# Kernel optimization log

Hardware: AMD Instinct MI355X
Metric: run time of the kernel (lower is better)

The kernel has to match this reference:

```python
import jax, jax.numpy as jnp
import numpy as np

N_NODES = 100000
N_EDGES = 640000
D_IN = 128
D_HID = 128
D_OUT = 128
EPS = 1e-12  # F.normalize clamp_min eps


def _sage_conv(x, src, dst, Wl, bl, Wr):
    # mean aggregation of source features onto destination nodes
    msgs = x[src]                                              # [E, C] gather
    agg = jax.ops.segment_sum(msgs, dst, num_segments=N_NODES)  # [N, C] scatter-add
    cnt = jax.ops.segment_sum(jnp.ones((src.shape[0],), x.dtype), dst,
                              num_segments=N_NODES)
    agg = agg / jnp.maximum(cnt, 1.0)[:, None]
    out = agg @ Wl.T + bl + x @ Wr.T                           # lin_l(aggr) + lin_r(root)
    # L2 row-normalize (normalize=True)
    norm = jnp.sqrt(jnp.sum(out * out, axis=-1, keepdims=True))
    return out / jnp.maximum(norm, EPS)


def setup_inputs() -> dict:
    key = jax.random.key(0)
    ks = jax.random.split(key, 8)
    x = jax.random.normal(ks[0], (N_NODES, D_IN), dtype=jnp.float32)
    edge_index = jax.random.randint(ks[1], (2, N_EDGES), 0, N_NODES, dtype=jnp.int64)
    s1 = 1.0 / np.sqrt(D_IN)
    s2 = 1.0 / np.sqrt(D_HID)
    Wl1 = jax.random.uniform(ks[2], (D_HID, D_IN), jnp.float32, -s1, s1)
    bl1 = jax.random.uniform(ks[3], (D_HID,), jnp.float32, -s1, s1)
    Wr1 = jax.random.uniform(ks[4], (D_HID, D_IN), jnp.float32, -s1, s1)
    Wl2 = jax.random.uniform(ks[5], (D_OUT, D_HID), jnp.float32, -s2, s2)
    bl2 = jax.random.uniform(ks[6], (D_OUT,), jnp.float32, -s2, s2)
    Wr2 = jax.random.uniform(ks[7], (D_OUT, D_HID), jnp.float32, -s2, s2)
    return {"x": x, "edge_index": edge_index, "Wl1": Wl1, "bl1": bl1,
            "Wr1": Wr1, "Wl2": Wl2, "bl2": bl2, "Wr2": Wr2}


def reference(x, edge_index, Wl1, bl1, Wr1, Wl2, bl2, Wr2):
    src, dst = edge_index[0], edge_index[1]
    h = _sage_conv(x, src, dst, Wl1, bl1, Wr1)
    h = jax.nn.relu(h)  # dropout is identity in eval mode
    h = _sage_conv(h, src, dst, Wl2, bl2, Wr2)
    return h
```

## Files before the change

### kernel.cpp

```cpp
#include <hip/hip_runtime.h>
#include <hip/hip_bf16.h>
#include <stdint.h>

#define N_NODES 100000
#define N_EDGES 640000
#define MPAD    100096
#define CONV_T  (N_NODES * 64)
#define EDGE_BLOCKS ((N_EDGES + 255) / 256)

typedef short  bf8_t  __attribute__((ext_vector_type(8)));
typedef float  f32x4  __attribute__((ext_vector_type(4)));

__device__ __forceinline__ unsigned f2bf(float f) {
  unsigned u = __builtin_bit_cast(unsigned, f);
  return ((u + 0x7fffu + ((u >> 16) & 1u)) >> 16) & 0xffffu;
}
__device__ __forceinline__ float bf2f(unsigned bits) {
  return __builtin_bit_cast(float, bits << 16);
}

__global__ void k_count_prep(const int* __restrict__ dst, int* __restrict__ cnt,
                             const float* __restrict__ x, unsigned* __restrict__ A1,
                             const float* __restrict__ Wl1, const float* __restrict__ Wr1,
                             unsigned short* __restrict__ Bf1,
                             const float* __restrict__ Wl2, const float* __restrict__ Wr2,
                             unsigned short* __restrict__ Bf2) {
  if (blockIdx.x < EDGE_BLOCKS) {
    int e = blockIdx.x * 256 + threadIdx.x;
    if (e < N_EDGES) atomicAdd(&cnt[dst[e]], 1);
    return;
  }
  int i = (blockIdx.x - EDGE_BLOCKS) * 256 + threadIdx.x;
  if (i < CONV_T) {
    int w = i >> 6, lane = i & 63;
    float2 v = ((const float2*)x)[i];
    A1[(size_t)w * 128 + 64 + lane] = f2bf(v.x) | (f2bf(v.y) << 16);
    return;
  }
  int gid = i - CONV_T;
  if (gid >= 8192) return;
  int tid = gid & 4095;
  const float* Wl = (gid < 4096) ? Wl1 : Wl2;
  const float* Wr = (gid < 4096) ? Wr1 : Wr2;
  unsigned short* Bf = (gid < 4096) ? Bf1 : Bf2;
  int lane = tid & 63;
  int t  = (tid >> 6) & 7;
  int kc = tid >> 9;
  int c = lane & 15, q = lane >> 4;
  int col = t * 16 + c;
  for (int j = 0; j < 8; ++j) {
    int k = kc * 32 + q * 8 + j;
    float v = (k < 128) ? Wl[col * 128 + k] : Wr[col * 128 + (k - 128)];
    Bf[(size_t)tid * 8 + j] = (unsigned short)f2bf(v);
  }
}

__global__ void k_bsum(const int* __restrict__ cnt, int* __restrict__ bsum) {
  __shared__ int s[256];
  int base = blockIdx.x * 1024;
  int t = threadIdx.x;
  int v = 0;
  for (int j = 0; j < 4; ++j) {
    int i = base + j * 256 + t;
    if (i < N_NODES) v += cnt[i];
  }
  s[t] = v; __syncthreads();
  for (int o = 128; o > 0; o >>= 1) { if (t < o) s[t] += s[t + o]; __syncthreads(); }
  if (t == 0) bsum[blockIdx.x] = s[0];
}

__global__ void k_scanb(int* __restrict__ bsum, int nb) {
  __shared__ int s[128];
  int t = threadIdx.x;
  int v = (t < nb) ? bsum[t] : 0;
  s[t] = v; __syncthreads();
  for (int o = 1; o < 128; o <<= 1) {
    int add = (t >= o) ? s[t - o] : 0;
    __syncthreads();
    s[t] += add;
    __syncthreads();
  }
  if (t < nb) bsum[t] = s[t] - v;
}

__global__ void k_scanchunk(const int* __restrict__ cnt, const int* __restrict__ bsum,
                            int* __restrict__ rowptr, float* __restrict__ inv) {
  __shared__ int s[1024];
  int t = threadIdx.x;
  int i = blockIdx.x * 1024 + t;
  int v = (i < N_NODES) ? cnt[i] : 0;
  s[t] = v; __syncthreads();
  for (int o = 1; o < 1024; o <<= 1) {
    int add = (t >= o) ? s[t - o] : 0;
    __syncthreads();
    s[t] += add;
    __syncthreads();
  }
  int incl = s[t];
  int bofs = bsum[blockIdx.x];
  if (i < N_NODES) {
    rowptr[i] = bofs + incl - v;
    inv[i] = 1.0f / fmaxf((float)v, 1.0f);
  }
  if (i == N_NODES - 1) rowptr[N_NODES] = bofs + incl;
}

__global__ void k_scatter(const int* __restrict__ src, const int* __restrict__ dst,
                          const int* __restrict__ rowptr, int* __restrict__ cursor,
                          int* __restrict__ esrc) {
  int e = blockIdx.x * blockDim.x + threadIdx.x;
  if (e < N_EDGES) {
    int d = dst[e];
    int p = atomicAdd(&cursor[d], 1);
    esrc[rowptr[d] + p] = src[e];
  }
}

__global__ __launch_bounds__(256) void k_agg(const unsigned* __restrict__ A,
    const int* __restrict__ rowptr, const int* __restrict__ esrc,
    const float* __restrict__ inv) {
  int w = (blockIdx.x * blockDim.x + threadIdx.x) >> 6;
  int lane = threadIdx.x & 63;
  if (w >= N_NODES) return;
  int b = rowptr[w], e = rowptr[w + 1];
  int deg = e - b;
  int myi = (lane < deg) ? esrc[b + lane] : 0;
  float ax = 0.f, ay = 0.f;
  int n = (deg < 64) ? deg : 64;
  for (int j0 = 0; j0 < n; j0 += 8) {
    unsigned u[8];
#pragma unroll
    for (int j = 0; j < 8; ++j) {
      int s = __shfl(myi, j0 + j);
      u[j] = A[(size_t)s * 128 + 64 + lane];
    }
#pragma unroll
    for (int j = 0; j < 8; ++j) {
      if (j0 + j < n) { ax += bf2f(u[j] & 0xffffu); ay += bf2f(u[j] >> 16); }
    }
  }
  for (int j = b + 64; j < e; ++j) {
    int s = esrc[j];
    unsigned u = A[(size_t)s * 128 + 64 + lane];
    ax += bf2f(u & 0xffffu); ay += bf2f(u >> 16);
  }
  float iv = inv[w];
  ((unsigned*)A)[(size_t)w * 128 + lane] = f2bf(ax * iv) | (f2bf(ay * iv) << 16);
}

template<int LAYER>
__global__ __launch_bounds__(256) void k_gemm(const unsigned short* __restrict__ A,
    const unsigned short* __restrict__ Bf, const float* __restrict__ bias,
    void* __restrict__ outp) {
  __shared__ unsigned short Bs[32768];
  int wid = threadIdx.x >> 6;
  int lane = threadIdx.x & 63;
  int c = lane & 15, q = lane >> 4;
  int m0 = blockIdx.x * 128 + wid * 32;

  bf8_t a0[8], a1[8];
#pragma unroll
  for (int kc = 0; kc < 8; ++kc) {
    a0[kc] = *(const bf8_t*)(A + (size_t)(m0 + c) * 256 + kc * 32 + q * 8);
    a1[kc] = *(const bf8_t*)(A + (size_t)(m0 + 16 + c) * 256 + kc * 32 + q * 8);
  }
#pragma unroll
  for (int i = 0; i < 16; ++i)
    ((bf8_t*)Bs)[i * 256 + threadIdx.x] = ((const bf8_t*)Bf)[i * 256 + threadIdx.x];
  __syncthreads();

  f32x4 acc[2][8];
#pragma unroll
  for (int h = 0; h < 2; ++h)
#pragma unroll
    for (int t = 0; t < 8; ++t) acc[h][t] = (f32x4){0.f, 0.f, 0.f, 0.f};
  const bf8_t* Bv = (const bf8_t*)Bs;
#pragma unroll
  for (int kc = 0; kc < 8; ++kc) {
#pragma unroll
    for (int t = 0; t < 8; ++t) {
      bf8_t b = Bv[(kc * 8 + t) * 64 + lane];
      acc[0][t] = __builtin_amdgcn_mfma_f32_16x16x32_bf16(a0[kc], b, acc[0][t], 0, 0, 0);
      acc[1][t] = __builtin_amdgcn_mfma_f32_16x16x32_bf16(a1[kc], b, acc[1][t], 0, 0, 0);
    }
  }
  float bcol[8];
#pragma unroll
  for (int t = 0; t < 8; ++t) bcol[t] = bias[t * 16 + c];
#pragma unroll
  for (int h = 0; h < 2; ++h) {
#pragma unroll
    for (int r = 0; r < 4; ++r) {
      float ss = 0.f;
#pragma unroll
      for (int t = 0; t < 8; ++t) {
        float v = acc[h][t][r] + bcol[t];
        acc[h][t][r] = v;
        ss += v * v;
      }
#pragma unroll
      for (int m = 1; m < 16; m <<= 1) ss += __shfl_xor(ss, m, 64);
      float invn = 1.0f / fmaxf(sqrtf(ss), 1e-12f);
      int row = m0 + h * 16 + q * 4 + r;
      if (LAYER == 1) {
        unsigned* o32 = (unsigned*)outp;
#pragma unroll
        for (int t = 0; t < 8; ++t) {
          float v = fmaxf(acc[h][t][r] * invn, 0.f);
          float vp = __shfl_xor(v, 1, 64);
          if (row < N_NODES && !(c & 1))
            o32[(size_t)row * 128 + 64 + t * 8 + (c >> 1)] = f2bf(v) | (f2bf(vp) << 16);
        }
      } else {
        float* o = (float*)outp;
        if (row < N_NODES) {
#pragma unroll
          for (int t = 0; t < 8; ++t)
            o[(size_t)row * 128 + t * 16 + c] = acc[h][t][r] * invn;
        }
      }
    }
  }
}

extern "C" void kernel_launch(void* const* d_in, const int* in_sizes, int n_in,
                              void* d_out, int out_size, void* d_ws, size_t ws_size,
                              hipStream_t stream) {
  const float* x   = (const float*)d_in[0];
  const int*   ei  = (const int*)d_in[1];
  const int*   src = ei;
  const int*   dst = ei + N_EDGES;
  const float* Wl1 = (const float*)d_in[2];
  const float* bl1 = (const float*)d_in[3];
  const float* Wr1 = (const float*)d_in[4];
  const float* Wl2 = (const float*)d_in[5];
  const float* bl2 = (const float*)d_in[6];
  const float* Wr2 = (const float*)d_in[7];

  char* ws = (char*)d_ws;
  size_t off = 0;
  auto alloc = [&](size_t bytes) -> void* {
    void* p = ws + off;
    off += (bytes + 255) & ~(size_t)255;
    return p;
  };
  unsigned short* A1  = (unsigned short*)alloc((size_t)MPAD * 256 * 2);
  unsigned short* A2  = (unsigned short*)alloc((size_t)MPAD * 256 * 2);
  unsigned short* Bf1 = (unsigned short*)alloc(65536);
  unsigned short* Bf2 = (unsigned short*)alloc(65536);
  int*   esrc   = (int*)alloc((size_t)N_EDGES * 4);
  int*   rowptr = (int*)alloc((size_t)(N_NODES + 1) * 4);
  int*   cnt    = (int*)alloc((size_t)N_NODES * 4);
  int*   cursor = (int*)alloc((size_t)N_NODES * 4);
  float* inv    = (float*)alloc((size_t)N_NODES * 4);
  int*   bsum   = (int*)alloc(1024);

  const size_t cntR = ((size_t)N_NODES * 4 + 255) & ~(size_t)255;
  hipMemsetAsync(cnt, 0, 2 * cntR, stream);

  const int NB = (N_NODES + 1023) / 1024;
  const int PREP_BLOCKS = (CONV_T + 8192 + 255) / 256;
  k_count_prep<<<EDGE_BLOCKS + PREP_BLOCKS, 256, 0, stream>>>(
                 dst, cnt, x, (unsigned*)A1, Wl1, Wr1, Bf1, Wl2, Wr2, Bf2);
  k_bsum     <<<NB, 256, 0, stream>>>(cnt, bsum);
  k_scanb    <<<1, 128, 0, stream>>>(bsum, NB);
  k_scanchunk<<<NB, 1024, 0, stream>>>(cnt, bsum, rowptr, inv);
  k_scatter  <<<(N_EDGES + 255) / 256, 256, 0, stream>>>(src, dst, rowptr, cursor, esrc);

  k_agg    <<<(N_NODES * 64 + 255) / 256, 256, 0, stream>>>((unsigned*)A1, rowptr, esrc, inv);
  k_gemm<1><<<MPAD / 128, 256, 0, stream>>>(A1, Bf1, bl1, A2);
  k_agg    <<<(N_NODES * 64 + 255) / 256, 256, 0, stream>>>((unsigned*)A2, rowptr, esrc, inv);
  k_gemm<2><<<MPAD / 128, 256, 0, stream>>>(A2, Bf2, bl2, d_out);
}
```

Before: 299.5 us.

## Vectorize aggregation with half-wave edges and move prep into scatter kernel

The aggregation kernel now has each half-wave load 8-byte chunks of a neighbour row, so one wave processes two edges per load with wider accesses, and the two halves are combined with a cross-lane shuffle. The feature conversion and weight packing move out of the counting kernel into the scatter kernel and use float4 loads. The cursor array is now zeroed inside the scan kernel, which shrinks the memset. This is meant to raise memory-level parallelism in the gather and cut per-element work in the bf16 conversion, at the cost of an extra reduction shuffle and some idle lanes for odd-degree nodes.

```diff
diff --git a/kernel.cpp b/kernel.cpp
--- a/kernel.cpp
+++ b/kernel.cpp
@@ -5,8 +5,9 @@
 #define N_NODES 100000
 #define N_EDGES 640000
 #define MPAD    100096
-#define CONV_T  (N_NODES * 64)
 #define EDGE_BLOCKS ((N_EDGES + 255) / 256)
+#define CONV4_T     (N_NODES * 32)
+#define CONV4_BLOCKS ((CONV4_T + 255) / 256)
 
 typedef short  bf8_t  __attribute__((ext_vector_type(8)));
 typedef float  f32x4  __attribute__((ext_vector_type(4)));
@@ -19,25 +20,94 @@
   return __builtin_bit_cast(float, bits << 16);
 }
 
-__global__ void k_count_prep(const int* __restrict__ dst, int* __restrict__ cnt,
-                             const float* __restrict__ x, unsigned* __restrict__ A1,
-                             const float* __restrict__ Wl1, const float* __restrict__ Wr1,
-                             unsigned short* __restrict__ Bf1,
-                             const float* __restrict__ Wl2, const float* __restrict__ Wr2,
-                             unsigned short* __restrict__ Bf2) {
-  if (blockIdx.x < EDGE_BLOCKS) {
-    int e = blockIdx.x * 256 + threadIdx.x;
-    if (e < N_EDGES) atomicAdd(&cnt[dst[e]], 1);
+__global__ void k_count(const int* __restrict__ dst, int* __restrict__ cnt) {
+  int e = blockIdx.x * blockDim.x + threadIdx.x;
+  if (e < N_EDGES) atomicAdd(&cnt[dst[e]], 1);
+}
+
+__global__ void k_bsum(const int* __restrict__ cnt, int* __restrict__ bsum) {
+  __shared__ int s[256];
+  int base = blockIdx.x * 1024;
+  int t = threadIdx.x;
+  int v = 0;
+  for (int j = 0; j < 4; ++j) {
+    int i = base + j * 256 + t;
+    if (i < N_NODES) v += cnt[i];
+  }
+  s[t] = v; __syncthreads();
+  for (int o = 128; o > 0; o >>= 1) { if (t < o) s[t] += s[t + o]; __syncthreads(); }
+  if (t == 0) bsum[blockIdx.x] = s[0];
+}
+
+__global__ void k_scanb(int* __restrict__ bsum, int nb) {
+  __shared__ int s[128];
+  int t = threadIdx.x;
+  int v = (t < nb) ? bsum[t] : 0;
+  s[t] = v; __syncthreads();
+  for (int o = 1; o < 128; o <<= 1) {
+    int add = (t >= o) ? s[t - o] : 0;
+    __syncthreads();
+    s[t] += add;
+    __syncthreads();
+  }
+  if (t < nb) bsum[t] = s[t] - v;
+}
+
+__global__ void k_scanchunk(const int* __restrict__ cnt, const int* __restrict__ bsum,
+                            int* __restrict__ rowptr, float* __restrict__ inv,
+                            int* __restrict__ cursor) {
+  __shared__ int s[1024];
+  int t = threadIdx.x;
+  int i = blockIdx.x * 1024 + t;
+  int v = (i < N_NODES) ? cnt[i] : 0;
+  s[t] = v; __syncthreads();
+  for (int o = 1; o < 1024; o <<= 1) {
+    int add = (t >= o) ? s[t - o] : 0;
+    __syncthreads();
+    s[t] += add;
+    __syncthreads();
+  }
+  int incl = s[t];
+  int bofs = bsum[blockIdx.x];
+  if (i < N_NODES) {
+    rowptr[i] = bofs + incl - v;
+    inv[i] = 1.0f / fmaxf((float)v, 1.0f);
+    cursor[i] = 0;
+  }
+  if (i == N_NODES - 1) rowptr[N_NODES] = bofs + incl;
+}
+
+__global__ void k_scatter_prep(const int* __restrict__ src, const int* __restrict__ dst,
+                               const int* __restrict__ rowptr, int* __restrict__ cursor,
+                               int* __restrict__ esrc,
+                               const float* __restrict__ x, unsigned* __restrict__ A1,
+                               const float* __restrict__ Wl1, const float* __restrict__ Wr1,
+                               unsigned short* __restrict__ Bf1,
+                               const float* __restrict__ Wl2, const float* __restrict__ Wr2,
+                               unsigned short* __restrict__ Bf2) {
+  int bx = blockIdx.x;
+  if (bx < EDGE_BLOCKS) {
+    int e = bx * 256 + threadIdx.x;
+    if (e < N_EDGES) {
+      int d = dst[e];
+      int p = atomicAdd(&cursor[d], 1);
+      esrc[rowptr[d] + p] = src[e];
+    }
     return;
   }
-  int i = (blockIdx.x - EDGE_BLOCKS) * 256 + threadIdx.x;
-  if (i < CONV_T) {
-    int w = i >> 6, lane = i & 63;
-    float2 v = ((const float2*)x)[i];
-    A1[(size_t)w * 128 + 64 + lane] = f2bf(v.x) | (f2bf(v.y) << 16);
+  if (bx < EDGE_BLOCKS + CONV4_BLOCKS) {
+    int i = (bx - EDGE_BLOCKS) * 256 + threadIdx.x;
+    if (i < CONV4_T) {
+      int w = i >> 5, t = i & 31;
+      float4 f = ((const float4*)x)[i];
+      uint2 u;
+      u.x = f2bf(f.x) | (f2bf(f.y) << 16);
+      u.y = f2bf(f.z) | (f2bf(f.w) << 16);
+      ((uint2*)A1)[(size_t)w * 64 + 32 + t] = u;
+    }
     return;
   }
-  int gid = i - CONV_T;
+  int gid = (bx - EDGE_BLOCKS - CONV4_BLOCKS) * 256 + threadIdx.x;
   if (gid >= 8192) return;
   int tid = gid & 4095;
   const float* Wl = (gid < 4096) ? Wl1 : Wl2;
@@ -55,68 +125,7 @@
   }
 }
 
-__global__ void k_bsum(const int* __restrict__ cnt, int* __restrict__ bsum) {
-  __shared__ int s[256];
-  int base = blockIdx.x * 1024;
-  int t = threadIdx.x;
-  int v = 0;
-  for (int j = 0; j < 4; ++j) {
-    int i = base + j * 256 + t;
-    if (i < N_NODES) v += cnt[i];
-  }
-  s[t] = v; __syncthreads();
-  for (int o = 128; o > 0; o >>= 1) { if (t < o) s[t] += s[t + o]; __syncthreads(); }
-  if (t == 0) bsum[blockIdx.x] = s[0];
-}
-
-__global__ void k_scanb(int* __restrict__ bsum, int nb) {
-  __shared__ int s[128];
-  int t = threadIdx.x;
-  int v = (t < nb) ? bsum[t] : 0;
-  s[t] = v; __syncthreads();
-  for (int o = 1; o < 128; o <<= 1) {
-    int add = (t >= o) ? s[t - o] : 0;
-    __syncthreads();
-    s[t] += add;
-    __syncthreads();
-  }
-  if (t < nb) bsum[t] = s[t] - v;
-}
-
-__global__ void k_scanchunk(const int* __restrict__ cnt, const int* __restrict__ bsum,
-                            int* __restrict__ rowptr, float* __restrict__ inv) {
-  __shared__ int s[1024];
-  int t = threadIdx.x;
-  int i = blockIdx.x * 1024 + t;
-  int v = (i < N_NODES) ? cnt[i] : 0;
-  s[t] = v; __syncthreads();
-  for (int o = 1; o < 1024; o <<= 1) {
-    int add = (t >= o) ? s[t - o] : 0;
-    __syncthreads();
-    s[t] += add;
-    __syncthreads();
-  }
-  int incl = s[t];
-  int bofs = bsum[blockIdx.x];
-  if (i < N_NODES) {
-    rowptr[i] = bofs + incl - v;
-    inv[i] = 1.0f / fmaxf((float)v, 1.0f);
-  }
-  if (i == N_NODES - 1) rowptr[N_NODES] = bofs + incl;
-}
-
-__global__ void k_scatter(const int* __restrict__ src, const int* __restrict__ dst,
-                          const int* __restrict__ rowptr, int* __restrict__ cursor,
-                          int* __restrict__ esrc) {
-  int e = blockIdx.x * blockDim.x + threadIdx.x;
-  if (e < N_EDGES) {
-    int d = dst[e];
-    int p = atomicAdd(&cursor[d], 1);
-    esrc[rowptr[d] + p] = src[e];
-  }
-}
-
-__global__ __launch_bounds__(256) void k_agg(const unsigned* __restrict__ A,
+__global__ __launch_bounds__(256) void k_agg(unsigned* __restrict__ A,
     const int* __restrict__ rowptr, const int* __restrict__ esrc,
     const float* __restrict__ inv) {
   int w = (blockIdx.x * blockDim.x + threadIdx.x) >> 6;
@@ -125,27 +134,44 @@
   int b = rowptr[w], e = rowptr[w + 1];
   int deg = e - b;
   int myi = (lane < deg) ? esrc[b + lane] : 0;
-  float ax = 0.f, ay = 0.f;
+  int half = lane >> 5, l32 = lane & 31;
+  const uint2* Av = (const uint2*)A;
+  float ax = 0.f, ay = 0.f, az = 0.f, aw = 0.f;
   int n = (deg < 64) ? deg : 64;
-  for (int j0 = 0; j0 < n; j0 += 8) {
-    unsigned u[8];
-#pragma unroll
-    for (int j = 0; j < 8; ++j) {
-      int s = __shfl(myi, j0 + j);
-      u[j] = A[(size_t)s * 128 + 64 + lane];
-    }
-#pragma unroll
-    for (int j = 0; j < 8; ++j) {
-      if (j0 + j < n) { ax += bf2f(u[j] & 0xffffu); ay += bf2f(u[j] >> 16); }
-    }
-  }
-  for (int j = b + 64; j < e; ++j) {
-    int s = esrc[j];
-    unsigned u = A[(size_t)s * 128 + 64 + lane];
-    ax += bf2f(u & 0xffffu); ay += bf2f(u >> 16);
-  }
+  for (int j0 = 0; j0 < n; j0 += 16) {
+    uint2 u[8];
+#pragma unroll
+    for (int jj = 0; jj < 8; ++jj) {
+      int slot = j0 + jj * 2 + half;
+      int s = __shfl(myi, slot);
+      u[jj] = Av[(size_t)s * 64 + 32 + l32];
+    }
+#pragma unroll
+    for (int jj = 0; jj < 8; ++jj) {
+      if (j0 + jj * 2 + half < n) {
+        ax += bf2f(u[jj].x & 0xffffu); ay += bf2f(u[jj].x >> 16);
+        az += bf2f(u[jj].y & 0xffffu); aw += bf2f(u[jj].y >> 16);
+      }
+    }
+  }
+  for (int j = 64; j < deg; j += 2) {
+    int slot = j + half;
+    int s = (slot < deg) ? esrc[b + slot] : 0;
+    uint2 u = Av[(size_t)s * 64 + 32 + l32];
+    if (slot < deg) {
+      ax += bf2f(u.x & 0xffffu); ay += bf2f(u.x >> 16);
+      az += bf2f(u.y & 0xffffu); aw += bf2f(u.y >> 16);
+    }
+  }
+  ax += __shfl_xor(ax, 32, 64); ay += __shfl_xor(ay, 32, 64);
+  az += __shfl_xor(az, 32, 64); aw += __shfl_xor(aw, 32, 64);
   float iv = inv[w];
-  ((unsigned*)A)[(size_t)w * 128 + lane] = f2bf(ax * iv) | (f2bf(ay * iv) << 16);
+  if (half == 0) {
+    uint2 o;
+    o.x = f2bf(ax * iv) | (f2bf(ay * iv) << 16);
+    o.y = f2bf(az * iv) | (f2bf(aw * iv) << 16);
+    ((uint2*)A)[(size_t)w * 64 + l32] = o;
+  }
 }
 
 template<int LAYER>
@@ -255,17 +281,16 @@
   float* inv    = (float*)alloc((size_t)N_NODES * 4);
   int*   bsum   = (int*)alloc(1024);
 
-  const size_t cntR = ((size_t)N_NODES * 4 + 255) & ~(size_t)255;
-  hipMemsetAsync(cnt, 0, 2 * cntR, stream);
+  hipMemsetAsync(cnt, 0, (size_t)N_NODES * 4, stream);
 
   const int NB = (N_NODES + 1023) / 1024;
-  const int PREP_BLOCKS = (CONV_T + 8192 + 255) / 256;
-  k_count_prep<<<EDGE_BLOCKS + PREP_BLOCKS, 256, 0, stream>>>(
-                 dst, cnt, x, (unsigned*)A1, Wl1, Wr1, Bf1, Wl2, Wr2, Bf2);
-  k_bsum     <<<NB, 256, 0, stream>>>(cnt, bsum);
-  k_scanb    <<<1, 128, 0, stream>>>(bsum, NB);
-  k_scanchunk<<<NB, 1024, 0, stream>>>(cnt, bsum, rowptr, inv);
-  k_scatter  <<<(N_EDGES + 255) / 256, 256, 0, stream>>>(src, dst, rowptr, cursor, esrc);
+  k_count      <<<EDGE_BLOCKS, 256, 0, stream>>>(dst, cnt);
+  k_bsum       <<<NB, 256, 0, stream>>>(cnt, bsum);
+  k_scanb      <<<1, 128, 0, stream>>>(bsum, NB);
+  k_scanchunk  <<<NB, 1024, 0, stream>>>(cnt, bsum, rowptr, inv, cursor);
+  k_scatter_prep<<<EDGE_BLOCKS + CONV4_BLOCKS + 32, 256, 0, stream>>>(
+                 src, dst, rowptr, cursor, esrc,
+                 x, (unsigned*)A1, Wl1, Wr1, Bf1, Wl2, Wr2, Bf2);
 
   k_agg    <<<(N_NODES * 64 + 255) / 256, 256, 0, stream>>>((unsigned*)A1, rowptr, esrc, inv);
   k_gemm<1><<<MPAD / 128, 256, 0, stream>>>(A1, Bf1, bl1, A2);
```

New measurement: 304.6 us. No clear change (+1.7%).
